# Kernel optimization log

Measured on AMD Instinct MI355X. Metric: run time of the kernel, lower is better.

The kernel has to match this reference:

```python
import jax, jax.numpy as jnp
import numpy as np
import math

V = 32000; SMAX = 256; N = 512; M = 16; TICKS = 4; D = 512
NSA = 256; NSO = 512; H = 8; HD = D // H; B = 2; S = 256


def _ln(x, g, b, eps=1e-5):
    m = x.mean(-1, keepdims=True)
    v = ((x - m) ** 2).mean(-1, keepdims=True)
    return (x - m) / jnp.sqrt(v + eps) * g + b


def _glu(x):
    a, b = jnp.split(x, 2, axis=-1)
    return a * jax.nn.sigmoid(b)


def setup_inputs() -> dict:
    key = jax.random.key(0)
    ks = iter(jax.random.split(key, 64))
    rn = lambda shape, s: jax.random.normal(next(ks), shape, jnp.float32) * s
    inp = {}
    inp['x'] = jax.random.randint(next(ks), (B, S), 0, V)
    inp['tok_table'] = rn((V, D), 0.02)
    inp['pos_embed'] = rn((SMAX, D), 0.02)
    inp['ln_emb_g'] = jnp.ones(D); inp['ln_emb_b'] = jnp.zeros(D)
    inp['kv_w'] = rn((D, D), 1 / math.sqrt(D)); inp['kv_b'] = jnp.zeros(D)
    inp['kv_ln_g'] = jnp.ones(D); inp['kv_ln_b'] = jnp.zeros(D)
    inp['q_w'] = rn((NSA, D), 1 / math.sqrt(NSA)); inp['q_b'] = jnp.zeros(D)
    inp['wq'] = rn((D, D), 1 / math.sqrt(D)); inp['bq'] = jnp.zeros(D)
    inp['wk'] = rn((D, D), 1 / math.sqrt(D)); inp['bk'] = jnp.zeros(D)
    inp['wv'] = rn((D, D), 1 / math.sqrt(D)); inp['bv'] = jnp.zeros(D)
    inp['ow'] = rn((D, D), 1 / math.sqrt(D)); inp['ob'] = jnp.zeros(D)
    inp['syn_w'] = rn((D + N, 2 * N), 1 / math.sqrt(D + N)); inp['syn_b'] = jnp.zeros(2 * N)
    inp['syn_g'] = jnp.ones(N); inp['syn_beta'] = jnp.zeros(N)
    inp['fc1_w'] = rn((N, M, 256), math.sqrt(2.0 / M)); inp['fc1_b'] = jnp.zeros((N, 256))
    inp['fc2_w'] = rn((N, 128, 2), math.sqrt(2.0 / 128)); inp['fc2_b'] = jnp.zeros((N, 2))
    inp['nlm_T'] = jnp.ones(1)
    a = math.sqrt(1.0 / N)
    inp['start_act'] = jax.random.uniform(next(ks), (SMAX, N), jnp.float32, -a, a)
    b2 = math.sqrt(1.0 / (N + M))
    inp['start_trace'] = jax.random.uniform(next(ks), (SMAX, N, M), jnp.float32, -b2, b2)
    inp['decay_a'] = jnp.zeros(NSA); inp['decay_o'] = jnp.zeros(NSO)
    inp['out_w'] = rn((NSO, V), 1 / math.sqrt(NSO)); inp['out_b'] = jnp.zeros(V)
    inp['idx_al'] = jax.random.randint(next(ks), (NSA,), 0, N)
    inp['idx_ar'] = jax.random.randint(next(ks), (NSA,), 0, N)
    inp['idx_ol'] = jax.random.randint(next(ks), (NSO,), 0, N)
    inp['idx_or'] = jax.random.randint(next(ks), (NSO,), 0, N)
    return inp


def reference(x, tok_table, pos_embed, ln_emb_g, ln_emb_b, kv_w, kv_b, kv_ln_g, kv_ln_b,
              q_w, q_b, wq, bq, wk, bk, wv, bv, ow, ob, syn_w, syn_b, syn_g, syn_beta,
              fc1_w, fc1_b, fc2_w, fc2_b, nlm_T, start_act, start_trace, decay_a, decay_o,
              out_w, out_b, idx_al, idx_ar, idx_ol, idx_or):
    Bz, Sl = x.shape
    emb = _ln(tok_table[x] + pos_embed[:Sl], ln_emb_g, ln_emb_b)        # (B,S,D)
    kv = _ln(emb @ kv_w + kv_b, kv_ln_g, kv_ln_b)
    k = (kv @ wk + bk).reshape(Bz, Sl, H, HD)                            # keys/values fixed over ticks
    v = (kv @ wv + bv).reshape(Bz, Sl, H, HD)
    mask = jnp.triu(jnp.ones((Sl, Sl), bool), 1)                         # True = masked
    r_a = jnp.exp(-decay_a)
    r_o = jnp.exp(-decay_o)
    act = jnp.broadcast_to(start_act[:Sl], (Bz, Sl, N))
    trace = jnp.broadcast_to(start_trace[:Sl], (Bz, Sl, N, M))
    aa = ba = ao_ = bo = None
    preds, certs = [], []
    for _ in range(TICKS):
        # action synchronization (decayed pairwise product)
        pp = act[:, :, idx_al] * act[:, :, idx_ar]
        if aa is None:
            aa, ba = pp, jnp.ones_like(pp)
        else:
            aa, ba = r_a * aa + pp, r_a * ba + 1.0
        sync_a = aa / jnp.sqrt(ba + 1e-8)
        # causal attention with query from action sync
        qh = ((sync_a @ q_w + q_b) @ wq + bq).reshape(Bz, Sl, H, HD)
        sc = jnp.einsum('bqhd,bkhd->bhqk', qh, k) / math.sqrt(HD)
        sc = jnp.where(mask, -1e9, sc)
        attn_out = jnp.einsum('bhqk,bkhd->bqhd', jax.nn.softmax(sc, -1), v).reshape(Bz, Sl, D) @ ow + ob
        # synapse MLP -> new pre-activation, shift memory trace
        state = _ln(_glu(jnp.concatenate([attn_out, act], -1) @ syn_w + syn_b), syn_g, syn_beta)
        trace = jnp.concatenate([trace[..., 1:], state[..., None]], -1)
        # per-neuron NLM (batched private GEMMs)
        h = _glu(jnp.einsum('bsnm,nmh->bsnh', trace, fc1_w) + fc1_b)
        o = _glu(jnp.einsum('bsnh,nho->bsno', h, fc2_w) + fc2_b)
        act = o[..., 0] / nlm_T[0]
        # output synchronization + prediction
        ppo = act[:, :, idx_ol] * act[:, :, idx_or]
        if ao_ is None:
            ao_, bo = ppo, jnp.ones_like(ppo)
        else:
            ao_, bo = r_o * ao_ + ppo, r_o * bo + 1.0
        pred = (ao_ / jnp.sqrt(bo + 1e-8)) @ out_w + out_b                # (B,S,V)
        p = jax.nn.softmax(pred, -1)
        ent = -(p * jnp.log(p + 1e-10)).sum(-1) / math.log(V)
        preds.append(pred)
        certs.append(jnp.stack([ent, 1.0 - ent], -1))
    return jnp.stack(preds, -1), jnp.stack(certs, -1)
```

## Files before the change

kernel.cpp:

```cpp
#include <hip/hip_runtime.h>
#include <cstdint>
#include <cstddef>

#define BATCH 2
#define SEQ   256
#define DIM   512
#define NN    512
#define MM    16
#define NTICK 4
#define NSA   256
#define NSO   512
#define NHEAD 8
#define HDIM  64
#define VOCAB 32000
#define BS    (BATCH*SEQ)
#define NBLK  500

typedef __bf16 bf16;
typedef bf16  bf16x4  __attribute__((ext_vector_type(4)));
typedef bf16  bf16x8v __attribute__((ext_vector_type(8)));
typedef float f32x4   __attribute__((ext_vector_type(4)));

typedef __attribute__((address_space(1))) const void av1_t;
typedef __attribute__((address_space(3))) void av3_t;

__global__ __launch_bounds__(128) void embed_kernel(const int* __restrict__ x,
    const float* __restrict__ tok, const float* __restrict__ pos, float* __restrict__ out){
  int row = blockIdx.x;
  int s = row & (SEQ-1);
  int token = x[row];
  const float4* tr = (const float4*)(tok + (size_t)token*DIM);
  const float4* pr = (const float4*)(pos + (size_t)s*DIM);
  float4* orow = (float4*)(out + (size_t)row*DIM);
  for (int i = threadIdx.x; i < DIM/4; i += blockDim.x){
    float4 a = tr[i], b = pr[i];
    float4 o; o.x=a.x+b.x; o.y=a.y+b.y; o.z=a.z+b.z; o.w=a.w+b.w;
    orow[i] = o;
  }
}

__global__ __launch_bounds__(256) void ln512_kernel(const float* __restrict__ in,
    const float* __restrict__ g, const float* __restrict__ b, float* __restrict__ out){
  int row = blockIdx.x, tid = threadIdx.x;
  const float* xr = in + (size_t)row*512;
  float v0 = xr[tid], v1 = xr[tid+256];
  float s = v0+v1, ss = v0*v0+v1*v1;
  #pragma unroll
  for (int o = 32; o > 0; o >>= 1){ s += __shfl_down(s, o); ss += __shfl_down(ss, o); }
  __shared__ float rs[4], rss[4];
  __shared__ float smean, sinv;
  int wid = tid >> 6, lane = tid & 63;
  if (lane == 0){ rs[wid] = s; rss[wid] = ss; }
  __syncthreads();
  if (tid == 0){
    float S = rs[0]+rs[1]+rs[2]+rs[3];
    float SS = rss[0]+rss[1]+rss[2]+rss[3];
    float m = S * (1.0f/512.0f);
    float var = SS * (1.0f/512.0f) - m*m;
    smean = m; sinv = 1.0f/sqrtf(var + 1e-5f);
  }
  __syncthreads();
  float m = smean, inv = sinv;
  out[(size_t)row*512 + tid]       = (v0-m)*inv*g[tid]     + b[tid];
  out[(size_t)row*512 + tid + 256] = (v1-m)*inv*g[tid+256] + b[tid+256];
}

__global__ __launch_bounds__(256) void glu_ln_kernel(const float* __restrict__ y,
    const float* __restrict__ g, const float* __restrict__ beta, float* __restrict__ out){
  int row = blockIdx.x, tid = threadIdx.x;
  const float* yr = y + (size_t)row*1024;
  float a0 = yr[tid],     b0 = yr[tid+512];
  float a1 = yr[tid+256], b1 = yr[tid+768];
  float g0 = a0 / (1.0f + expf(-b0));
  float g1 = a1 / (1.0f + expf(-b1));
  float s = g0+g1, ss = g0*g0+g1*g1;
  #pragma unroll
  for (int o = 32; o > 0; o >>= 1){ s += __shfl_down(s, o); ss += __shfl_down(ss, o); }
  __shared__ float rs[4], rss[4];
  __shared__ float smean, sinv;
  int wid = tid >> 6, lane = tid & 63;
  if (lane == 0){ rs[wid] = s; rss[wid] = ss; }
  __syncthreads();
  if (tid == 0){
    float S = rs[0]+rs[1]+rs[2]+rs[3];
    float SS = rss[0]+rss[1]+rss[2]+rss[3];
    float m = S * (1.0f/512.0f);
    float var = SS * (1.0f/512.0f) - m*m;
    smean = m; sinv = 1.0f/sqrtf(var + 1e-5f);
  }
  __syncthreads();
  float m = smean, inv = sinv;
  out[(size_t)row*512 + tid]       = (g0-m)*inv*g[tid]     + beta[tid];
  out[(size_t)row*512 + tid + 256] = (g1-m)*inv*g[tid+256] + beta[tid+256];
}

__global__ __launch_bounds__(256) void sync_kernel(const float* __restrict__ act,
    const int* __restrict__ il, const int* __restrict__ ir, const float* __restrict__ decay,
    float* __restrict__ accA, float* __restrict__ accB,
    float* __restrict__ outf, bf16* __restrict__ outb, int NS, int first){
  int i = blockIdx.x*256 + threadIdx.x;
  if (i >= BS*NS) return;
  int bs = i / NS, c = i - bs*NS;
  const float* ar = act + (size_t)bs*NN;
  float p = ar[il[c]] * ar[ir[c]];
  float A, Bv;
  if (first){ A = p; Bv = 1.0f; }
  else {
    float r = expf(-decay[c]);
    A = r*accA[i] + p;
    Bv = r*accB[i] + 1.0f;
  }
  accA[i] = A; accB[i] = Bv;
  float sy = A / sqrtf(Bv + 1e-8f);
  if (outf) outf[i] = sy;
  if (outb) outb[i] = (bf16)sy;
}

__global__ __launch_bounds__(256) void split_t(const float* __restrict__ W,
    bf16* __restrict__ hiT, bf16* __restrict__ loT, int K, int N){
  __shared__ float t[32][33];
  int n0 = blockIdx.x*32, k0 = blockIdx.y*32;
  int tid = threadIdx.x;
  int r = tid >> 3, c4 = (tid & 7)*4;
  float4 v = *(const float4*)(W + (size_t)(k0+r)*N + n0 + c4);
  t[r][c4+0]=v.x; t[r][c4+1]=v.y; t[r][c4+2]=v.z; t[r][c4+3]=v.w;
  __syncthreads();
  bf16x4 hi, lo;
  #pragma unroll
  for (int j = 0; j < 4; j++){
    float a = t[c4+j][r];
    bf16 h = (bf16)a;
    hi[j] = h;
    lo[j] = (bf16)(a - (float)h);
  }
  *(bf16x4*)(hiT + (size_t)(n0+r)*K + k0 + c4) = hi;
  if (loT) *(bf16x4*)(loT + (size_t)(n0+r)*K + k0 + c4) = lo;
}

__global__ __launch_bounds__(64) void gemm_x3(
    const float* __restrict__ A, const bf16* __restrict__ WhT,
    const bf16* __restrict__ WlT, const float* __restrict__ bias,
    float* __restrict__ C, int K, int lda, int ldc){
  int n0 = blockIdx.x * 64, m0 = blockIdx.y * 16;
  int lane = threadIdx.x;
  int ln = lane & 15, kq = lane >> 4;
  f32x4 acc[4];
  #pragma unroll
  for (int nf = 0; nf < 4; nf++) acc[nf] = (f32x4){0.f,0.f,0.f,0.f};
  const float* arow = A + (size_t)(m0 + ln)*lda + kq*8;
  const bf16* w0h = WhT + (size_t)(n0 + ln)*K + kq*8;
  const bf16* w0l = WlT + (size_t)(n0 + ln)*K + kq*8;
  size_t nstep = (size_t)16*K;
  for (int k0 = 0; k0 < K; k0 += 32){
    float4 a0 = *(const float4*)(arow + k0);
    float4 a1 = *(const float4*)(arow + k0 + 4);
    float av[8] = {a0.x,a0.y,a0.z,a0.w,a1.x,a1.y,a1.z,a1.w};
    bf16x8v ahi, alo;
    #pragma unroll
    for (int j = 0; j < 8; j++){
      bf16 h = (bf16)av[j];
      ahi[j] = h;
      alo[j] = (bf16)(av[j] - (float)h);
    }
    #pragma unroll
    for (int nf = 0; nf < 4; nf++){
      bf16x8v bh = *(const bf16x8v*)(w0h + nf*nstep + k0);
      bf16x8v bl = *(const bf16x8v*)(w0l + nf*nstep + k0);
      acc[nf] = __builtin_amdgcn_mfma_f32_16x16x32_bf16(ahi, bh, acc[nf], 0,0,0);
      acc[nf] = __builtin_amdgcn_mfma_f32_16x16x32_bf16(alo, bh, acc[nf], 0,0,0);
      acc[nf] = __builtin_amdgcn_mfma_f32_16x16x32_bf16(ahi, bl, acc[nf], 0,0,0);
    }
  }
  #pragma unroll
  for (int nf = 0; nf < 4; nf++){
    int col = n0 + nf*16 + ln;
    float bb = bias ? bias[col] : 0.0f;
    #pragma unroll
    for (int r = 0; r < 4; r++)
      C[(size_t)(m0 + kq*4 + r)*ldc + col] = acc[nf][r] + bb;
  }
}

__global__ void qbc_kernel(const float* __restrict__ qb, const float* __restrict__ wq,
                           const float* __restrict__ bq, float* __restrict__ qbc){
  int j = blockIdx.x*64 + threadIdx.x;
  float s = bq[j];
  for (int k = 0; k < DIM; k++) s = fmaf(qb[k], wq[(size_t)k*DIM + j], s);
  qbc[j] = s;
}

__global__ __launch_bounds__(256) void attn_kernel(const float* __restrict__ qh,
    const float* __restrict__ kb, const float* __restrict__ vb, float* __restrict__ outb){
  int qt = blockIdx.x, h = blockIdx.y, b = blockIdx.z;
  __shared__ float qs[16][HDIM];
  __shared__ float sc[16][SEQ + 4];
  __shared__ float red[16][16];
  __shared__ float rowm[16], rowz[16];
  int tid = threadIdx.x;
  {
    int r = tid >> 4, c4 = tid & 15;
    *(float4*)&qs[r][c4*4] =
      *(const float4*)(qh + ((size_t)(b*SEQ + qt*16 + r))*DIM + h*HDIM + c4*4);
  }
  __syncthreads();
  {
    int kk = tid;
    const float* krow = kb + ((size_t)(b*SEQ + kk))*DIM + h*HDIM;
    float s[16] = {};
    for (int d4 = 0; d4 < HDIM/4; d4++){
      float4 k4 = *(const float4*)(krow + d4*4);
      #pragma unroll
      for (int q = 0; q < 16; q++){
        float4 q4 = *(const float4*)&qs[q][d4*4];
        s[q] += q4.x*k4.x + q4.y*k4.y + q4.z*k4.z + q4.w*k4.w;
      }
    }
    #pragma unroll
    for (int q = 0; q < 16; q++){
      int qg = qt*16 + q;
      sc[q][kk] = (kk > qg) ? -1e9f : s[q]*0.125f;
    }
  }
  __syncthreads();
  {
    int q = tid >> 4, seg = tid & 15;
    float m = -1e30f;
    for (int i = 0; i < 16; i++) m = fmaxf(m, sc[q][seg*16+i]);
    red[q][seg] = m;
  }
  __syncthreads();
  if (tid < 16){
    float m = red[tid][0];
    for (int i = 1; i < 16; i++) m = fmaxf(m, red[tid][i]);
    rowm[tid] = m;
  }
  __syncthreads();
  {
    int q = tid >> 4, seg = tid & 15;
    float m = rowm[q], z = 0.0f;
    for (int i = 0; i < 16; i++){
      float e = expf(sc[q][seg*16+i] - m);
      sc[q][seg*16+i] = e;
      z += e;
    }
    red[q][seg] = z;
  }
  __syncthreads();
  if (tid < 16){
    float z = 0.0f;
    for (int i = 0; i < 16; i++) z += red[tid][i];
    rowz[tid] = 1.0f / z;
  }
  __syncthreads();
  {
    int q = tid >> 4, dc = tid & 15;
    float inv = rowz[q];
    float ax=0, ay=0, az=0, aw=0;
    for (int kk = 0; kk < SEQ; kk++){
      float p = sc[q][kk];
      float4 v4 = *(const float4*)(vb + ((size_t)(b*SEQ + kk))*DIM + h*HDIM + dc*4);
      ax = fmaf(p, v4.x, ax); ay = fmaf(p, v4.y, ay);
      az = fmaf(p, v4.z, az); aw = fmaf(p, v4.w, aw);
    }
    float4 o; o.x=ax*inv; o.y=ay*inv; o.z=az*inv; o.w=aw*inv;
    *(float4*)(outb + ((size_t)(b*SEQ + qt*16 + q))*DIM + h*HDIM + dc*4) = o;
  }
}

__global__ void act_init_kernel(const float* __restrict__ sa, float* __restrict__ act){
  int i = blockIdx.x*256 + threadIdx.x;
  act[i] = sa[i & (SEQ*NN - 1)];
}
__global__ void cat_act_kernel(const float* __restrict__ act, float* __restrict__ cat){
  int i = blockIdx.x*256 + threadIdx.x;
  int bs = i >> 9, n = i & 511;
  cat[(size_t)bs*1024 + 512 + n] = act[i];
}

__global__ __launch_bounds__(256) void nlm_kernel(
    const float* __restrict__ start_trace,
    const float* __restrict__ s0, const float* __restrict__ s1,
    const float* __restrict__ s2, const float* __restrict__ s3,
    const float* __restrict__ fc1w, const float* __restrict__ fc1b,
    const float* __restrict__ fc2w, const float* __restrict__ fc2b,
    const float* __restrict__ nlmT, float* __restrict__ act, int t){
  int n = blockIdx.x, b = blockIdx.y, s = threadIdx.x;
  int bs = b*SEQ + s;
  size_t sidx = (size_t)bs*NN + n;
  float tr[16];
  #pragma unroll
  for (int j = 0; j < 16; j++){
    int src = j + t + 1;
    if (src < 16){
      tr[j] = start_trace[((size_t)s*NN + n)*MM + src];
    } else {
      int k = src - 16;
      tr[j] = (k==0) ? s0[sidx] : (k==1) ? s1[sidx] : (k==2) ? s2[sidx] : s3[sidx];
    }
  }
  const float* w1 = fc1w + (size_t)n*16*256;
  const float* b1 = fc1b + (size_t)n*256;
  const float* w2 = fc2w + (size_t)n*256;
  float o0 = fc2b[n*2+0], o1 = fc2b[n*2+1];
  #pragma unroll 4
  for (int j = 0; j < 128; j++){
    float a  = b1[j];
    float bb = b1[j+128];
    #pragma unroll
    for (int m = 0; m < 16; m++){
      a  = fmaf(tr[m], w1[m*256 + j],       a);
      bb = fmaf(tr[m], w1[m*256 + j + 128], bb);
    }
    float gg = a / (1.0f + expf(-bb));
    o0 = fmaf(gg, w2[j*2+0], o0);
    o1 = fmaf(gg, w2[j*2+1], o1);
  }
  float o = o0 / (1.0f + expf(-o1));
  act[sidx] = o / nlmT[0];
}

__global__ __launch_bounds__(256) void out_gemm3(
    const bf16* __restrict__ sy0, const bf16* __restrict__ sy1,
    const bf16* __restrict__ sy2, const bf16* __restrict__ sy3,
    const bf16* __restrict__ WoT, const float* __restrict__ bo,
    float* __restrict__ outp, float* __restrict__ pm,
    float* __restrict__ pz, float* __restrict__ ps){
  __shared__ bf16 Bs[64*512];
  int tid = threadIdx.x;
  int w = tid >> 6, lane = tid & 63;
  int ln = lane & 15, kq = lane >> 4;
  int n0 = blockIdx.x * 64;

  {
    const char* gp = (const char*)(WoT + (size_t)n0*512);
    char* lp = (char*)Bs;
    #pragma unroll
    for (int it = 0; it < 16; ++it){
      int ub = (w*16 + it) << 10;
      int b  = ub + lane*16;
      int src = b ^ (((b >> 10) & 7) << 4);
      __builtin_amdgcn_global_load_lds((av1_t*)(gp + src), (av3_t*)(lp + ub),
                                       16, 0, 0);
    }
  }
  __syncthreads();

  float bb[4];
  #pragma unroll
  for (int nf = 0; nf < 4; ++nf) bb[nf] = bo[n0 + nf*16 + ln];

  const size_t aoff = (size_t)ln*512 + (size_t)kq*8;
  const char* Bsc = (const char*)Bs;
  const int bbase = (ln << 10) + (kq << 4);
  const int sw = (ln & 7) << 4;

  for (int i = 0; i < 8; ++i){
    int m0 = w*16 + i*64;
    const bf16* pa0 = sy0 + (size_t)m0*512 + aoff;
    const bf16* pa1 = sy1 + (size_t)m0*512 + aoff;
    const bf16* pa2 = sy2 + (size_t)m0*512 + aoff;
    const bf16* pa3 = sy3 + (size_t)m0*512 + aoff;
    f32x4 acc[4][4];
    #pragma unroll
    for (int t = 0; t < 4; ++t)
      #pragma unroll
      for (int nf = 0; nf < 4; ++nf) acc[t][nf] = (f32x4){0.f,0.f,0.f,0.f};

    #pragma unroll
    for (int k0 = 0; k0 < 512; k0 += 32){
      bf16x8v a0 = *(const bf16x8v*)(pa0 + k0);
      bf16x8v a1 = *(const bf16x8v*)(pa1 + k0);
      bf16x8v a2 = *(const bf16x8v*)(pa2 + k0);
      bf16x8v a3 = *(const bf16x8v*)(pa3 + k0);
      int kb = bbase + k0*2;
      bf16x8v b0 = *(const bf16x8v*)(Bsc + ((kb           ) ^ sw));
      bf16x8v b1 = *(const bf16x8v*)(Bsc + ((kb + 16*1024) ^ sw));
      bf16x8v b2 = *(const bf16x8v*)(Bsc + ((kb + 32*1024) ^ sw));
      bf16x8v b3 = *(const bf16x8v*)(Bsc + ((kb + 48*1024) ^ sw));
      acc[0][0] = __builtin_amdgcn_mfma_f32_16x16x32_bf16(a0, b0, acc[0][0], 0,0,0);
      acc[1][0] = __builtin_amdgcn_mfma_f32_16x16x32_bf16(a1, b0, acc[1][0], 0,0,0);
      acc[2][0] = __builtin_amdgcn_mfma_f32_16x16x32_bf16(a2, b0, acc[2][0], 0,0,0);
      acc[3][0] = __builtin_amdgcn_mfma_f32_16x16x32_bf16(a3, b0, acc[3][0], 0,0,0);
      acc[0][1] = __builtin_amdgcn_mfma_f32_16x16x32_bf16(a0, b1, acc[0][1], 0,0,0);
      acc[1][1] = __builtin_amdgcn_mfma_f32_16x16x32_bf16(a1, b1, acc[1][1], 0,0,0);
      acc[2][1] = __builtin_amdgcn_mfma_f32_16x16x32_bf16(a2, b1, acc[2][1], 0,0,0);
      acc[3][1] = __builtin_amdgcn_mfma_f32_16x16x32_bf16(a3, b1, acc[3][1], 0,0,0);
      acc[0][2] = __builtin_amdgcn_mfma_f32_16x16x32_bf16(a0, b2, acc[0][2], 0,0,0);
      acc[1][2] = __builtin_amdgcn_mfma_f32_16x16x32_bf16(a1, b2, acc[1][2], 0,0,0);
      acc[2][2] = __builtin_amdgcn_mfma_f32_16x16x32_bf16(a2, b2, acc[2][2], 0,0,0);
      acc[3][2] = __builtin_amdgcn_mfma_f32_16x16x32_bf16(a3, b2, acc[3][2], 0,0,0);
      acc[0][3] = __builtin_amdgcn_mfma_f32_16x16x32_bf16(a0, b3, acc[0][3], 0,0,0);
      acc[1][3] = __builtin_amdgcn_mfma_f32_16x16x32_bf16(a1, b3, acc[1][3], 0,0,0);
      acc[2][3] = __builtin_amdgcn_mfma_f32_16x16x32_bf16(a2, b3, acc[2][3], 0,0,0);
      acc[3][3] = __builtin_amdgcn_mfma_f32_16x16x32_bf16(a3, b3, acc[3][3], 0,0,0);
    }

    #pragma unroll
    for (int t = 0; t < 4; ++t)
      #pragma unroll
      for (int nf = 0; nf < 4; ++nf)
        #pragma unroll
        for (int r = 0; r < 4; ++r) acc[t][nf][r] += bb[nf];

    #pragma unroll
    for (int r = 0; r < 4; ++r){
      size_t rowoff = (size_t)(m0 + kq*4 + r)*VOCAB;
      #pragma unroll
      for (int nf = 0; nf < 4; ++nf){
        float4 o;
        o.x = acc[0][nf][r]; o.y = acc[1][nf][r];
        o.z = acc[2][nf][r]; o.w = acc[3][nf][r];
        *(float4*)(outp + (rowoff + n0 + nf*16 + ln)*4) = o;
      }
    }

    #pragma unroll
    for (int t = 0; t < 4; ++t){
      #pragma unroll
      for (int r = 0; r < 4; ++r){
        float m = fmaxf(fmaxf(acc[t][0][r], acc[t][1][r]),
                        fmaxf(acc[t][2][r], acc[t][3][r]));
        #pragma unroll
        for (int o2 = 1; o2 < 16; o2 <<= 1) m = fmaxf(m, __shfl_xor(m, o2));
        float z = 0.0f, s = 0.0f;
        #pragma unroll
        for (int nf = 0; nf < 4; ++nf){
          float v = acc[t][nf][r] - m;
          float e = expf(v);
          z += e; s += v*e;
        }
        #pragma unroll
        for (int o2 = 1; o2 < 16; o2 <<= 1){ z += __shfl_xor(z, o2); s += __shfl_xor(s, o2); }
        if (ln == 0){
          size_t p = ((size_t)(m0 + kq*4 + r)*4 + t)*NBLK + blockIdx.x;
          pm[p] = m; pz[p] = z; ps[p] = s;
        }
      }
    }
  }
}

__global__ __launch_bounds__(64) void ent_final(const float* __restrict__ pm,
    const float* __restrict__ pz, const float* __restrict__ ps, float* __restrict__ certs){
  int row = blockIdx.x >> 2, t = blockIdx.x & 3;
  const size_t base = ((size_t)row*4 + t)*NBLK;
  int lane = threadIdx.x;
  float M = -1e30f, Z = 0.0f, S = 0.0f;
  for (int i = lane; i < NBLK; i += 64){
    float m2 = pm[base+i], z2 = pz[base+i], s2 = ps[base+i];
    float Mn = fmaxf(M, m2);
    float e1 = expf(M - Mn), e2 = expf(m2 - Mn);
    S = (S + (M - Mn)*Z)*e1 + (s2 + (m2 - Mn)*z2)*e2;
    Z = Z*e1 + z2*e2;
    M = Mn;
  }
  #pragma unroll
  for (int o = 1; o < 64; o <<= 1){
    float m2 = __shfl_xor(M, o), z2 = __shfl_xor(Z, o), s2 = __shfl_xor(S, o);
    float Mn = fmaxf(M, m2);
    float e1 = expf(M - Mn), e2 = expf(m2 - Mn);
    S = (S + (M - Mn)*Z)*e1 + (s2 + (m2 - Mn)*z2)*e2;
    Z = Z*e1 + z2*e2;
    M = Mn;
  }
  if (lane == 0){
    float ent = (logf(Z) - S/Z) * (1.0f / logf((float)VOCAB));
    certs[((size_t)row*2 + 0)*4 + t] = ent;
    certs[((size_t)row*2 + 1)*4 + t] = 1.0f - ent;
  }
}

extern "C" void kernel_launch(void* const* d_in, const int* in_sizes, int n_in,
                              void* d_out, int out_size, void* d_ws, size_t ws_size,
                              hipStream_t stream){
  const int*   x        = (const int*)  d_in[0];
  const float* tok      = (const float*)d_in[1];
  const float* pos      = (const float*)d_in[2];
  const float* ln_emb_g = (const float*)d_in[3];
  const float* ln_emb_b = (const float*)d_in[4];
  const float* kv_w     = (const float*)d_in[5];
  const float* kv_b     = (const float*)d_in[6];
  const float* kv_ln_g  = (const float*)d_in[7];
  const float* kv_ln_b  = (const float*)d_in[8];
  const float* q_w      = (const float*)d_in[9];
  const float* q_b      = (const float*)d_in[10];
  const float* wq       = (const float*)d_in[11];
  const float* bq       = (const float*)d_in[12];
  const float* wk       = (const float*)d_in[13];
  const float* bk       = (const float*)d_in[14];
  const float* wv       = (const float*)d_in[15];
  const float* bv       = (const float*)d_in[16];
  const float* ow       = (const float*)d_in[17];
  const float* ob       = (const float*)d_in[18];
  const float* syn_w    = (const float*)d_in[19];
  const float* syn_b    = (const float*)d_in[20];
  const float* syn_g    = (const float*)d_in[21];
  const float* syn_beta = (const float*)d_in[22];
  const float* fc1_w    = (const float*)d_in[23];
  const float* fc1_b    = (const float*)d_in[24];
  const float* fc2_w    = (const float*)d_in[25];
  const float* fc2_b    = (const float*)d_in[26];
  const float* nlm_T    = (const float*)d_in[27];
  const float* start_act   = (const float*)d_in[28];
  const float* start_trace = (const float*)d_in[29];
  const float* decay_a  = (const float*)d_in[30];
  const float* decay_o  = (const float*)d_in[31];
  const float* out_w    = (const float*)d_in[32];
  const float* out_b    = (const float*)d_in[33];
  const int* idx_al = (const int*)d_in[34];
  const int* idx_ar = (const int*)d_in[35];
  const int* idx_ol = (const int*)d_in[36];
  const int* idx_or = (const int*)d_in[37];

  char* wp = (char*)d_ws;
  auto alloc = [&](size_t bytes) -> void* {
    void* p = (void*)wp;
    wp += (bytes + 255) & ~(size_t)255;
    return p;
  };
  float* qwc      = (float*)alloc((size_t)256*512*4);
  float* qbc      = (float*)alloc(512*4);
  float* emb_raw  = (float*)alloc((size_t)BS*512*4);
  float* emb      = (float*)alloc((size_t)BS*512*4);
  float* kvt      = (float*)alloc((size_t)BS*512*4);
  float* kvn      = (float*)alloc((size_t)BS*512*4);
  float* kbuf     = (float*)alloc((size_t)BS*512*4);
  float* vbuf     = (float*)alloc((size_t)BS*512*4);
  float* act      = (float*)alloc((size_t)BS*512*4);
  float* aaB      = (float*)alloc((size_t)BS*256*4);
  float* baB      = (float*)alloc((size_t)BS*256*4);
  float* aoB      = (float*)alloc((size_t)BS*512*4);
  float* boB      = (float*)alloc((size_t)BS*512*4);
  float* sync_a   = (float*)alloc((size_t)BS*256*4);
  float* qh       = (float*)alloc((size_t)BS*512*4);
  float* attn_raw = (float*)alloc((size_t)BS*512*4);
  float* catb     = (float*)alloc((size_t)BS*1024*4);
  float* syn_y    = (float*)alloc((size_t)BS*1024*4);
  float* states[NTICK];
  for (int t = 0; t < NTICK; t++) states[t] = (float*)alloc((size_t)BS*512*4);
  bf16* syob[NTICK];
  for (int t = 0; t < NTICK; t++) syob[t] = (bf16*)alloc((size_t)BS*512*2);
  bf16* kvT_h = (bf16*)alloc((size_t)512*512*2);
  bf16* kvT_l = (bf16*)alloc((size_t)512*512*2);
  bf16* wkT_h = (bf16*)alloc((size_t)512*512*2);
  bf16* wkT_l = (bf16*)alloc((size_t)512*512*2);
  bf16* wvT_h = (bf16*)alloc((size_t)512*512*2);
  bf16* wvT_l = (bf16*)alloc((size_t)512*512*2);
  bf16* owT_h = (bf16*)alloc((size_t)512*512*2);
  bf16* owT_l = (bf16*)alloc((size_t)512*512*2);
  bf16* wqT_h = (bf16*)alloc((size_t)512*512*2);
  bf16* wqT_l = (bf16*)alloc((size_t)512*512*2);
  bf16* synT_h = (bf16*)alloc((size_t)1024*1024*2);
  bf16* synT_l = (bf16*)alloc((size_t)1024*1024*2);
  bf16* qwcT_h = (bf16*)alloc((size_t)512*256*2);
  bf16* qwcT_l = (bf16*)alloc((size_t)512*256*2);
  bf16* WoT    = (bf16*)alloc((size_t)VOCAB*512*2);
  float* pm = (float*)alloc((size_t)BS*4*NBLK*4);
  float* pz = (float*)alloc((size_t)BS*4*NBLK*4);
  float* ps = (float*)alloc((size_t)BS*4*NBLK*4);

  float* preds = (float*)d_out;
  float* certs = (float*)d_out + (size_t)BS*VOCAB*NTICK;

  split_t<<<dim3(16,16), 256, 0, stream>>>(kv_w,  kvT_h, kvT_l, 512, 512);
  split_t<<<dim3(16,16), 256, 0, stream>>>(wk,    wkT_h, wkT_l, 512, 512);
  split_t<<<dim3(16,16), 256, 0, stream>>>(wv,    wvT_h, wvT_l, 512, 512);
  split_t<<<dim3(16,16), 256, 0, stream>>>(ow,    owT_h, owT_l, 512, 512);
  split_t<<<dim3(16,16), 256, 0, stream>>>(wq,    wqT_h, wqT_l, 512, 512);
  split_t<<<dim3(32,32), 256, 0, stream>>>(syn_w, synT_h, synT_l, 1024, 1024);
  split_t<<<dim3(VOCAB/32,16), 256, 0, stream>>>(out_w, WoT, nullptr, 512, VOCAB);

  embed_kernel<<<BS, 128, 0, stream>>>(x, tok, pos, emb_raw);
  ln512_kernel<<<BS, 256, 0, stream>>>(emb_raw, ln_emb_g, ln_emb_b, emb);
  gemm_x3<<<dim3(8,32), 64, 0, stream>>>(emb, kvT_h, kvT_l, kv_b, kvt, 512, 512, 512);
  ln512_kernel<<<BS, 256, 0, stream>>>(kvt, kv_ln_g, kv_ln_b, kvn);
  gemm_x3<<<dim3(8,32), 64, 0, stream>>>(kvn, wkT_h, wkT_l, bk, kbuf, 512, 512, 512);
  gemm_x3<<<dim3(8,32), 64, 0, stream>>>(kvn, wvT_h, wvT_l, bv, vbuf, 512, 512, 512);
  gemm_x3<<<dim3(8,16), 64, 0, stream>>>(q_w, wqT_h, wqT_l, nullptr, qwc, 512, 512, 512);
  split_t<<<dim3(16,8), 256, 0, stream>>>(qwc, qwcT_h, qwcT_l, 256, 512);
  qbc_kernel<<<8, 64, 0, stream>>>(q_b, wq, bq, qbc);
  act_init_kernel<<<(BS*NN)/256, 256, 0, stream>>>(start_act, act);

  for (int t = 0; t < NTICK; t++){
    sync_kernel<<<(BS*NSA)/256, 256, 0, stream>>>(act, idx_al, idx_ar, decay_a,
        aaB, baB, sync_a, nullptr, NSA, t==0);
    gemm_x3<<<dim3(8,32), 64, 0, stream>>>(sync_a, qwcT_h, qwcT_l, qbc, qh, 256, 256, 512);
    attn_kernel<<<dim3(16, NHEAD, BATCH), 256, 0, stream>>>(qh, kbuf, vbuf, attn_raw);
    gemm_x3<<<dim3(8,32), 64, 0, stream>>>(attn_raw, owT_h, owT_l, ob, catb, 512, 512, 1024);
    cat_act_kernel<<<(BS*NN)/256, 256, 0, stream>>>(act, catb);
    gemm_x3<<<dim3(16,32), 64, 0, stream>>>(catb, synT_h, synT_l, syn_b, syn_y, 1024, 1024, 1024);
    glu_ln_kernel<<<BS, 256, 0, stream>>>(syn_y, syn_g, syn_beta, states[t]);
    nlm_kernel<<<dim3(NN, BATCH), 256, 0, stream>>>(start_trace,
        states[0], states[1], states[2], states[3],
        fc1_w, fc1_b, fc2_w, fc2_b, nlm_T, act, t);
    sync_kernel<<<(BS*NSO)/256, 256, 0, stream>>>(act, idx_ol, idx_or, decay_o,
        aoB, boB, nullptr, syob[t], NSO, t==0);
  }

  out_gemm3<<<dim3(NBLK), 256, 0, stream>>>(
      syob[0], syob[1], syob[2], syob[3], WoT, out_b, preds, pm, pz, ps);
  ent_final<<<BS*4, 64, 0, stream>>>(pm, pz, ps, certs);
}
```

Before: 1.449 ms.

## Fuse embed with layernorm, fold cat into producers, widen output GEMM blocks

Merges the embedding add with the first layernorm so the raw embedding buffer is no longer written and re-read. Writes act into the concatenation buffer directly from act_init and nlm_kernel, which removes the per-tick cat kernel. Runs the output GEMM with 512 threads per block, each wave covering fewer row tiles, and replaces the single-lane partial-stat stores with one spread-out store per lane in a block-major layout, with ent_final reading the new strided layout. The risks are extra register pressure from the launch bounds and strided reads in ent_final.

```diff
diff --git a/kernel.cpp b/kernel.cpp
--- a/kernel.cpp
+++ b/kernel.cpp
@@ -24,19 +24,35 @@
 typedef __attribute__((address_space(1))) const void av1_t;
 typedef __attribute__((address_space(3))) void av3_t;
 
-__global__ __launch_bounds__(128) void embed_kernel(const int* __restrict__ x,
-    const float* __restrict__ tok, const float* __restrict__ pos, float* __restrict__ out){
-  int row = blockIdx.x;
+__global__ __launch_bounds__(256) void emb_ln_kernel(const int* __restrict__ x,
+    const float* __restrict__ tok, const float* __restrict__ pos,
+    const float* __restrict__ g, const float* __restrict__ b, float* __restrict__ out){
+  int row = blockIdx.x, tid = threadIdx.x;
   int s = row & (SEQ-1);
   int token = x[row];
-  const float4* tr = (const float4*)(tok + (size_t)token*DIM);
-  const float4* pr = (const float4*)(pos + (size_t)s*DIM);
-  float4* orow = (float4*)(out + (size_t)row*DIM);
-  for (int i = threadIdx.x; i < DIM/4; i += blockDim.x){
-    float4 a = tr[i], b = pr[i];
-    float4 o; o.x=a.x+b.x; o.y=a.y+b.y; o.z=a.z+b.z; o.w=a.w+b.w;
-    orow[i] = o;
-  }
+  const float* tr = tok + (size_t)token*DIM;
+  const float* pr = pos + (size_t)s*DIM;
+  float v0 = tr[tid]     + pr[tid];
+  float v1 = tr[tid+256] + pr[tid+256];
+  float sm = v0+v1, ss = v0*v0+v1*v1;
+  #pragma unroll
+  for (int o = 32; o > 0; o >>= 1){ sm += __shfl_down(sm, o); ss += __shfl_down(ss, o); }
+  __shared__ float rs[4], rss[4];
+  __shared__ float smean, sinv;
+  int wid = tid >> 6, lane = tid & 63;
+  if (lane == 0){ rs[wid] = sm; rss[wid] = ss; }
+  __syncthreads();
+  if (tid == 0){
+    float S = rs[0]+rs[1]+rs[2]+rs[3];
+    float SS = rss[0]+rss[1]+rss[2]+rss[3];
+    float m = S * (1.0f/512.0f);
+    float var = SS * (1.0f/512.0f) - m*m;
+    smean = m; sinv = 1.0f/sqrtf(var + 1e-5f);
+  }
+  __syncthreads();
+  float m = smean, inv = sinv;
+  out[(size_t)row*512 + tid]       = (v0-m)*inv*g[tid]     + b[tid];
+  out[(size_t)row*512 + tid + 256] = (v1-m)*inv*g[tid+256] + b[tid+256];
 }
 
 __global__ __launch_bounds__(256) void ln512_kernel(const float* __restrict__ in,
@@ -267,14 +283,13 @@
   }
 }
 
-__global__ void act_init_kernel(const float* __restrict__ sa, float* __restrict__ act){
+__global__ void act_init_kernel(const float* __restrict__ sa, float* __restrict__ act,
+                                float* __restrict__ catb){
   int i = blockIdx.x*256 + threadIdx.x;
-  act[i] = sa[i & (SEQ*NN - 1)];
-}
-__global__ void cat_act_kernel(const float* __restrict__ act, float* __restrict__ cat){
-  int i = blockIdx.x*256 + threadIdx.x;
+  float v = sa[i & (SEQ*NN - 1)];
+  act[i] = v;
   int bs = i >> 9, n = i & 511;
-  cat[(size_t)bs*1024 + 512 + n] = act[i];
+  catb[(size_t)bs*1024 + 512 + n] = v;
 }
 
 __global__ __launch_bounds__(256) void nlm_kernel(
@@ -283,7 +298,8 @@
     const float* __restrict__ s2, const float* __restrict__ s3,
     const float* __restrict__ fc1w, const float* __restrict__ fc1b,
     const float* __restrict__ fc2w, const float* __restrict__ fc2b,
-    const float* __restrict__ nlmT, float* __restrict__ act, int t){
+    const float* __restrict__ nlmT, float* __restrict__ act,
+    float* __restrict__ catb, int t){
   int n = blockIdx.x, b = blockIdx.y, s = threadIdx.x;
   int bs = b*SEQ + s;
   size_t sidx = (size_t)bs*NN + n;
@@ -316,10 +332,12 @@
     o1 = fmaf(gg, w2[j*2+1], o1);
   }
   float o = o0 / (1.0f + expf(-o1));
-  act[sidx] = o / nlmT[0];
-}
-
-__global__ __launch_bounds__(256) void out_gemm3(
+  float outv = o / nlmT[0];
+  act[sidx] = outv;
+  catb[(size_t)bs*1024 + 512 + n] = outv;
+}
+
+__global__ __launch_bounds__(512, 4) void out_gemm4(
     const bf16* __restrict__ sy0, const bf16* __restrict__ sy1,
     const bf16* __restrict__ sy2, const bf16* __restrict__ sy3,
     const bf16* __restrict__ WoT, const float* __restrict__ bo,
@@ -335,8 +353,8 @@
     const char* gp = (const char*)(WoT + (size_t)n0*512);
     char* lp = (char*)Bs;
     #pragma unroll
-    for (int it = 0; it < 16; ++it){
-      int ub = (w*16 + it) << 10;
+    for (int it = 0; it < 8; ++it){
+      int ub = (w*8 + it) << 10;
       int b  = ub + lane*16;
       int src = b ^ (((b >> 10) & 7) << 4);
       __builtin_amdgcn_global_load_lds((av1_t*)(gp + src), (av3_t*)(lp + ub),
@@ -353,9 +371,10 @@
   const char* Bsc = (const char*)Bs;
   const int bbase = (ln << 10) + (kq << 4);
   const int sw = (ln & 7) << 4;
-
-  for (int i = 0; i < 8; ++i){
-    int m0 = w*16 + i*64;
+  const int selt = ln & 3, selr = (ln >> 2) & 3;
+
+  for (int i = 0; i < 4; ++i){
+    int m0 = w*16 + i*128;
     const bf16* pa0 = sy0 + (size_t)m0*512 + aoff;
     const bf16* pa1 = sy1 + (size_t)m0*512 + aoff;
     const bf16* pa2 = sy2 + (size_t)m0*512 + aoff;
@@ -414,6 +433,7 @@
       }
     }
 
+    float mv = 0.f, zv = 0.f, sv = 0.f;
     #pragma unroll
     for (int t = 0; t < 4; ++t){
       #pragma unroll
@@ -431,23 +451,23 @@
         }
         #pragma unroll
         for (int o2 = 1; o2 < 16; o2 <<= 1){ z += __shfl_xor(z, o2); s += __shfl_xor(s, o2); }
-        if (ln == 0){
-          size_t p = ((size_t)(m0 + kq*4 + r)*4 + t)*NBLK + blockIdx.x;
-          pm[p] = m; pz[p] = z; ps[p] = s;
-        }
+        if (t == selt && r == selr){ mv = m; zv = z; sv = s; }
       }
     }
+    size_t p = ((size_t)blockIdx.x*512 + (m0 + kq*4 + selr))*4 + selt;
+    pm[p] = mv; pz[p] = zv; ps[p] = sv;
   }
 }
 
 __global__ __launch_bounds__(64) void ent_final(const float* __restrict__ pm,
     const float* __restrict__ pz, const float* __restrict__ ps, float* __restrict__ certs){
   int row = blockIdx.x >> 2, t = blockIdx.x & 3;
-  const size_t base = ((size_t)row*4 + t)*NBLK;
+  const size_t base = (size_t)row*4 + t;
   int lane = threadIdx.x;
   float M = -1e30f, Z = 0.0f, S = 0.0f;
   for (int i = lane; i < NBLK; i += 64){
-    float m2 = pm[base+i], z2 = pz[base+i], s2 = ps[base+i];
+    size_t idx = base + (size_t)i*2048;
+    float m2 = pm[idx], z2 = pz[idx], s2 = ps[idx];
     float Mn = fmaxf(M, m2);
     float e1 = expf(M - Mn), e2 = expf(m2 - Mn);
     S = (S + (M - Mn)*Z)*e1 + (s2 + (m2 - Mn)*z2)*e2;
@@ -520,7 +540,6 @@
   };
   float* qwc      = (float*)alloc((size_t)256*512*4);
   float* qbc      = (float*)alloc(512*4);
-  float* emb_raw  = (float*)alloc((size_t)BS*512*4);
   float* emb      = (float*)alloc((size_t)BS*512*4);
   float* kvt      = (float*)alloc((size_t)BS*512*4);
   float* kvn      = (float*)alloc((size_t)BS*512*4);
@@ -555,9 +574,9 @@
   bf16* qwcT_h = (bf16*)alloc((size_t)512*256*2);
   bf16* qwcT_l = (bf16*)alloc((size_t)512*256*2);
   bf16* WoT    = (bf16*)alloc((size_t)VOCAB*512*2);
-  float* pm = (float*)alloc((size_t)BS*4*NBLK*4);
-  float* pz = (float*)alloc((size_t)BS*4*NBLK*4);
-  float* ps = (float*)alloc((size_t)BS*4*NBLK*4);
+  float* pm = (float*)alloc((size_t)NBLK*512*4*4);
+  float* pz = (float*)alloc((size_t)NBLK*512*4*4);
+  float* ps = (float*)alloc((size_t)NBLK*512*4*4);
 
   float* preds = (float*)d_out;
   float* certs = (float*)d_out + (size_t)BS*VOCAB*NTICK;
@@ -570,8 +589,7 @@
   split_t<<<dim3(32,32), 256, 0, stream>>>(syn_w, synT_h, synT_l, 1024, 1024);
   split_t<<<dim3(VOCAB/32,16), 256, 0, stream>>>(out_w, WoT, nullptr, 512, VOCAB);
 
-  embed_kernel<<<BS, 128, 0, stream>>>(x, tok, pos, emb_raw);
-  ln512_kernel<<<BS, 256, 0, stream>>>(emb_raw, ln_emb_g, ln_emb_b, emb);
+  emb_ln_kernel<<<BS, 256, 0, stream>>>(x, tok, pos, ln_emb_g, ln_emb_b, emb);
   gemm_x3<<<dim3(8,32), 64, 0, stream>>>(emb, kvT_h, kvT_l, kv_b, kvt, 512, 512, 512);
   ln512_kernel<<<BS, 256, 0, stream>>>(kvt, kv_ln_g, kv_ln_b, kvn);
   gemm_x3<<<dim3(8,32), 64, 0, stream>>>(kvn, wkT_h, wkT_l, bk, kbuf, 512, 512, 512);
@@ -579,7 +597,7 @@
   gemm_x3<<<dim3(8,16), 64, 0, stream>>>(q_w, wqT_h, wqT_l, nullptr, qwc, 512, 512, 512);
   split_t<<<dim3(16,8), 256, 0, stream>>>(qwc, qwcT_h, qwcT_l, 256, 512);
   qbc_kernel<<<8, 64, 0, stream>>>(q_b, wq, bq, qbc);
-  act_init_kernel<<<(BS*NN)/256, 256, 0, stream>>>(start_act, act);
+  act_init_kernel<<<(BS*NN)/256, 256, 0, stream>>>(start_act, act, catb);
 
   for (int t = 0; t < NTICK; t++){
     sync_kernel<<<(BS*NSA)/256, 256, 0, stream>>>(act, idx_al, idx_ar, decay_a,
@@ -587,17 +605,16 @@
     gemm_x3<<<dim3(8,32), 64, 0, stream>>>(sync_a, qwcT_h, qwcT_l, qbc, qh, 256, 256, 512);
     attn_kernel<<<dim3(16, NHEAD, BATCH), 256, 0, stream>>>(qh, kbuf, vbuf, attn_raw);
     gemm_x3<<<dim3(8,32), 64, 0, stream>>>(attn_raw, owT_h, owT_l, ob, catb, 512, 512, 1024);
-    cat_act_kernel<<<(BS*NN)/256, 256, 0, stream>>>(act, catb);
     gemm_x3<<<dim3(16,32), 64, 0, stream>>>(catb, synT_h, synT_l, syn_b, syn_y, 1024, 1024, 1024);
     glu_ln_kernel<<<BS, 256, 0, stream>>>(syn_y, syn_g, syn_beta, states[t]);
     nlm_kernel<<<dim3(NN, BATCH), 256, 0, stream>>>(start_trace,
         states[0], states[1], states[2], states[3],
-        fc1_w, fc1_b, fc2_w, fc2_b, nlm_T, act, t);
+        fc1_w, fc1_b, fc2_w, fc2_b, nlm_T, act, catb, t);
     sync_kernel<<<(BS*NSO)/256, 256, 0, stream>>>(act, idx_ol, idx_or, decay_o,
         aoB, boB, nullptr, syob[t], NSO, t==0);
   }
 
-  out_gemm3<<<dim3(NBLK), 256, 0, stream>>>(
+  out_gemm4<<<dim3(NBLK), 512, 0, stream>>>(
       syob[0], syob[1], syob[2], syob[3], WoT, out_b, preds, pm, pz, ps);
   ent_final<<<BS*4, 64, 0, stream>>>(pm, pz, ps, certs);
 }
```

Measured after the change: 1.678 ms. 1.16x slower.
